# Kernel tuning notes

Hardware: AMD Instinct MI355X
Metric: run time of the kernel (lower is better)

## Reference

```python
import jax, jax.numpy as jnp
import numpy as np

N, L, E, H, D = 4, 2048, 1024, 16, 64

def setup_inputs() -> dict:
    key = jax.random.key(0)
    ks = jax.random.split(key, 8)
    s = 1.0 / np.sqrt(E)
    return {
        "Q": jax.random.normal(ks[0], (N, L, E), jnp.float32),
        "K": jax.random.normal(ks[1], (N, L, E), jnp.float32),
        "V": jax.random.normal(ks[2], (N, L, E), jnp.float32),
        "Wq": jax.random.normal(ks[3], (H * D, E), jnp.float32) * s,
        "bq": jnp.zeros((H * D,), jnp.float32),
        "Wk": jax.random.normal(ks[4], (H * D, E), jnp.float32) * s,
        "bk": jnp.zeros((H * D,), jnp.float32),
        "Wv": jax.random.normal(ks[5], (H * D, E), jnp.float32) * s,
        "bv": jnp.zeros((H * D,), jnp.float32),
        "Wo": jax.random.normal(ks[6], (E, H * D), jnp.float32) * s,
        "bo": jnp.zeros((E,), jnp.float32),
    }

def reference(Q, K, V, Wq, bq, Wk, bk, Wv, bv, Wo, bo):
    n, lq, e = Q.shape
    lk = K.shape[1]
    # projections: Linear(x) = x @ W.T + b
    q = (Q @ Wq.T + bq).reshape(n, lq, H, D)
    k = (K @ Wk.T + bk).reshape(n, lk, H, D)
    v = (V @ Wv.T + bv).reshape(n, lk, H, D)
    # scores over key dim (original broadcasts Q*K and sums over d)
    scores = jnp.einsum('nqhd,nkhd->nqkh', q, k) / jnp.sqrt(jnp.float32(D))
    attn = jax.nn.softmax(scores, axis=2)  # softmax over key axis
    out = jnp.einsum('nqkh,nkhd->nqhd', attn, v)
    out = out.reshape(n, lq, H * D)
    return (out @ Wo.T + bo).reshape(n, lq, E)
```

## Files before the change

### kernel.cpp

```cpp
#include <hip/hip_runtime.h>
#include <cstdint>
#include <cstddef>


typedef __bf16 bf16x8 __attribute__((ext_vector_type(8)));
typedef __bf16 bf16x4 __attribute__((ext_vector_type(4)));
typedef __bf16 bf16x2 __attribute__((ext_vector_type(2)));
typedef float f32x4 __attribute__((ext_vector_type(4)));
typedef float f32x2 __attribute__((ext_vector_type(2)));
typedef unsigned int uint2v __attribute__((ext_vector_type(2)));
typedef unsigned int uint4v __attribute__((ext_vector_type(4)));

#define LOG2E_OVER_SQRTD 0.18033688011112042f

__device__ __forceinline__ unsigned short f2bf(float f) {
  unsigned int u = __builtin_bit_cast(unsigned int, f);
  u = (u + 0x7fffu + ((u >> 16) & 1u)) >> 16;
  return (unsigned short)u;
}

__device__ __forceinline__ unsigned int pk2(float a, float b) {
  f32x2 t = {a, b};
  bf16x2 h = __builtin_convertvector(t, bf16x2);
  return __builtin_bit_cast(unsigned int, h);
}

__device__ __forceinline__ void gl2lds16(const void* g, void* l) {
  __builtin_amdgcn_global_load_lds(
      (__attribute__((address_space(1))) unsigned int*)g,
      (__attribute__((address_space(3))) unsigned int*)l, 16, 0, 0);
}

__device__ __forceinline__ bf16x8 mk_ap(f32x4 sA, f32x4 sB) {
  float peA[4], peB[4];
#pragma unroll
  for (int r = 0; r < 4; ++r) {
    peA[r] = __builtin_amdgcn_exp2f(sA[r]);
    peB[r] = __builtin_amdgcn_exp2f(sB[r]);
  }
  unsigned int x00 = pk2(peA[0], peA[1]);
  unsigned int x01 = pk2(peA[2], peA[3]);
  unsigned int x10 = pk2(peB[0], peB[1]);
  unsigned int x11 = pk2(peB[2], peB[3]);
  uint2v s0 = __builtin_amdgcn_permlane32_swap(x00, x10, false, false);
  uint2v t0 = __builtin_amdgcn_permlane16_swap(s0[0], s0[1], false, false);
  uint2v s1 = __builtin_amdgcn_permlane32_swap(x01, x11, false, false);
  uint2v t1 = __builtin_amdgcn_permlane16_swap(s1[0], s1[1], false, false);
  uint4v u;
  u[0] = t0[0];
  u[1] = t1[0];
  u[2] = t0[1];
  u[3] = t1[1];
  return __builtin_bit_cast(bf16x8, u);
}

struct CvtArgs {
  const float* src[7];
  unsigned short* dst[7];
};
__global__ __launch_bounds__(256) void cvt_all_k(CvtArgs a) {
  int bid = blockIdx.x;
  int which, x;
  if (bid < 24576) {
    which = bid >> 13;
    x = bid & 8191;
  } else {
    int r = bid - 24576;
    which = 3 + (r >> 10);
    x = r & 1023;
  }
  const float* s = a.src[which];
  unsigned short* d = a.dst[which];
  size_t i = ((size_t)x * 256 + threadIdx.x) * 4;
  float4 v = *(const float4*)(s + i);
  ushort4 o;
  o.x = f2bf(v.x); o.y = f2bf(v.y); o.z = f2bf(v.z); o.w = f2bf(v.w);
  *(ushort4*)(d + i) = o;
}

struct GemmDesc {
  const unsigned short* A;
  const unsigned short* Bt;
  const float* bias;
  void* C;
  int N;
  int nbx_shift;
  float scale;
  int bias_row;
  int permc;
};
struct GemmPack3 {
  GemmDesc g[3];
};

template <bool OUT_F32>
__global__ __launch_bounds__(256, 2) void gemm_multi_k(GemmPack3 p) {
  __shared__ __attribute__((aligned(16))) unsigned short As[128 * 64];
  __shared__ __attribute__((aligned(16))) unsigned short Bs[128 * 64];
  const GemmDesc d = p.g[blockIdx.x >> 9];
  const int t = blockIdx.x & 511;
  const int bx = t & ((1 << d.nbx_shift) - 1);
  const int by = t >> d.nbx_shift;

  const int tid = threadIdx.x;
  const int lane = tid & 63, wave = tid >> 6;
  const int lr = lane & 15, lg = lane >> 4;
  const int rowBase = by * 128;
  const int colBase = bx * 128;
  const int wm = (wave & 1) * 64, wn = (wave >> 1) * 64;

  f32x4 acc[4][4] = {};

  const unsigned short* gA[4];
  const unsigned short* gB[4];
  unsigned short* lA[4];
  unsigned short* lB[4];
#pragma unroll
  for (int i = 0; i < 4; ++i) {
    int s = tid + i * 256;
    int row = s >> 3;
    int c = (s & 7) ^ (row & 7);
    gA[i] = d.A + (size_t)(rowBase + row) * 1024 + c * 8;
    gB[i] = d.Bt + (size_t)(colBase + row) * 1024 + c * 8;
    lA[i] = &As[s * 8];
    lB[i] = &Bs[s * 8];
  }

  for (int kt = 0; kt < 16; ++kt) {
    const int ko = kt * 64;
#pragma unroll
    for (int i = 0; i < 4; ++i) {
      gl2lds16(gA[i] + ko, lA[i]);
      gl2lds16(gB[i] + ko, lB[i]);
    }
    __syncthreads();

#pragma unroll
    for (int ks = 0; ks < 2; ++ks) {
      bf16x8 af[4], bfr[4];
#pragma unroll
      for (int mt = 0; mt < 4; ++mt) {
        int row = wm + mt * 16 + lr;
        int c = (ks * 4 + lg) ^ (row & 7);
        af[mt] = *(const bf16x8*)&As[row * 64 + c * 8];
      }
#pragma unroll
      for (int nt = 0; nt < 4; ++nt) {
        int row = wn + nt * 16 + lr;
        int c = (ks * 4 + lg) ^ (row & 7);
        bfr[nt] = *(const bf16x8*)&Bs[row * 64 + c * 8];
      }
#pragma unroll
      for (int mt = 0; mt < 4; ++mt)
#pragma unroll
        for (int nt = 0; nt < 4; ++nt)
          acc[mt][nt] = __builtin_amdgcn_mfma_f32_16x16x32_bf16(
              af[mt], bfr[nt], acc[mt][nt], 0, 0, 0);
    }
    __syncthreads();
  }

#pragma unroll
  for (int mt = 0; mt < 4; ++mt)
#pragma unroll
    for (int nt = 0; nt < 4; ++nt) {
      int col = colBase + wn + nt * 16 + lr;
      int colStore = d.permc ? (colBase + wn + lr * 4 + nt) : col;
      float bcol = d.bias_row ? 0.f : d.bias[col];
#pragma unroll
      for (int r = 0; r < 4; ++r) {
        int row = rowBase + wm + mt * 16 + lg * 4 + r;
        float b = d.bias_row ? d.bias[row] : bcol;
        float val = (acc[mt][nt][r] + b) * d.scale;
        size_t idx = (size_t)row * (size_t)d.N + (size_t)colStore;
        if (OUT_F32)
          ((float*)d.C)[idx] = val;
        else
          ((unsigned short*)d.C)[idx] = f2bf(val);
      }
    }
}

__global__ __launch_bounds__(256, 4) void attn_k(
    const unsigned short* __restrict__ qb,
    const unsigned short* __restrict__ kb,
    const unsigned short* __restrict__ vtb,
    unsigned short* __restrict__ aob) {
  __shared__ __attribute__((aligned(16))) unsigned short Ks[2 * 64 * 64];
  __shared__ __attribute__((aligned(16))) unsigned short Vts[2 * 64 * 64];

  const int tid = threadIdx.x;
  const int lane = tid & 63, wave = tid >> 6;
  const int lr = lane & 15, lg = lane >> 4;

  const int bid = blockIdx.x;
  const int xcd = bid & 7;
  const int idx = bid >> 3;
  const int qt = idx & 15;
  const int nh = (idx >> 4) * 8 + xcd;
  const int h = nh & 15, n = nh >> 4;
  const int q0 = qt * 128;

#pragma unroll
  for (int i = 0; i < 4; ++i) {
    int s = i * 256 + tid;
    int row = s >> 3;
    int c = (s & 7) ^ (row & 7);
    gl2lds16(qb + (((size_t)n * 2048 + q0 + row) << 10) + h * 64 + c * 8,
             &Ks[s * 8]);
  }
  __syncthreads();

  bf16x8 aq[2][2];
#pragma unroll
  for (int mt = 0; mt < 2; ++mt)
#pragma unroll
    for (int ks = 0; ks < 2; ++ks) {
      int row = wave * 32 + mt * 16 + lr;
      int c = (ks * 4 + lg) ^ (row & 7);
      aq[mt][ks] = *(const bf16x8*)&Ks[row * 64 + c * 8];
    }
  __syncthreads();

  const int a0 = lr * 64 + ((lg ^ (lr & 7)) * 8);
  const int a1 = lr * 64 + (((4 + lg) ^ (lr & 7)) * 8);
  const unsigned short* Kb0 = &Ks[a0];
  const unsigned short* Kb1 = &Ks[a1];
  const unsigned short* Vb0 = &Vts[a0];
  const unsigned short* Vb1 = &Vts[a1];

  const unsigned short* kg[2];
  const unsigned short* vg[2];
  int ldo[2];
#pragma unroll
  for (int i = 0; i < 2; ++i) {
    int s = i * 256 + tid;
    int row = s >> 3;
    int c = (s & 7) ^ (row & 7);
    kg[i] = kb + (((size_t)n * 2048 + row) << 10) + h * 64 + c * 8;
    vg[i] = vtb + (((size_t)(h * 64 + row)) << 13) + (size_t)n * 2048 + c * 8;
    ldo[i] = s * 8;
  }
#pragma unroll
  for (int i = 0; i < 2; ++i) {
    gl2lds16(kg[i], &Ks[ldo[i]]);
    gl2lds16(vg[i], &Vts[ldo[i]]);
    kg[i] += 64 * 1024;
    vg[i] += 64;
  }

  bf16x8 ones;
#pragma unroll
  for (int i = 0; i < 8; ++i) ones[i] = (__bf16)1.0f;
  const f32x4 fzero = {0.f, 0.f, 0.f, 0.f};

  f32x4 o_acc[2][4] = {};
  f32x4 o_sum[2] = {};

#pragma unroll 2
  for (int kt = 0; kt < 32; ++kt) {
    const int cb = (kt & 1) * 4096;
    const int nb = 4096 - cb;
    __syncthreads();

    if (kt < 31) {
#pragma unroll
      for (int i = 0; i < 2; ++i) {
        gl2lds16(kg[i], &Ks[nb + ldo[i]]);
        gl2lds16(vg[i], &Vts[nb + ldo[i]]);
        kg[i] += 64 * 1024;
        vg[i] += 64;
      }
    }

    bf16x8 kf0[4], kf1[4];
#pragma unroll
    for (int nt = 0; nt < 4; ++nt) {
      kf0[nt] = *(const bf16x8*)(Kb0 + cb + nt * 1024);
      kf1[nt] = *(const bf16x8*)(Kb1 + cb + nt * 1024);
    }

    f32x4 sA[2][2], sB[2][2];
    __builtin_amdgcn_s_setprio(1);
#pragma unroll
    for (int mt = 0; mt < 2; ++mt)
#pragma unroll
      for (int nt = 0; nt < 2; ++nt) {
        f32x4 t0 = __builtin_amdgcn_mfma_f32_16x16x32_bf16(
            kf0[nt], aq[mt][0], fzero, 0, 0, 0);
        sA[mt][nt] = __builtin_amdgcn_mfma_f32_16x16x32_bf16(
            kf1[nt], aq[mt][1], t0, 0, 0, 0);
      }
#pragma unroll
    for (int mt = 0; mt < 2; ++mt)
#pragma unroll
      for (int nt = 0; nt < 2; ++nt) {
        f32x4 t0 = __builtin_amdgcn_mfma_f32_16x16x32_bf16(
            kf0[nt + 2], aq[mt][0], fzero, 0, 0, 0);
        sB[mt][nt] = __builtin_amdgcn_mfma_f32_16x16x32_bf16(
            kf1[nt + 2], aq[mt][1], t0, 0, 0, 0);
      }
    __builtin_amdgcn_s_setprio(0);

    bf16x8 bv0[4], bv1[4];
#pragma unroll
    for (int nt = 0; nt < 4; ++nt) {
      bv0[nt] = *(const bf16x8*)(Vb0 + cb + nt * 1024);
      bv1[nt] = *(const bf16x8*)(Vb1 + cb + nt * 1024);
    }

    bf16x8 ap0[2];
#pragma unroll
    for (int mt = 0; mt < 2; ++mt) ap0[mt] = mk_ap(sA[mt][0], sA[mt][1]);

    __builtin_amdgcn_s_setprio(1);
#pragma unroll
    for (int mt = 0; mt < 2; ++mt) {
      o_sum[mt] = __builtin_amdgcn_mfma_f32_16x16x32_bf16(
          ap0[mt], ones, o_sum[mt], 0, 0, 0);
#pragma unroll
      for (int nt = 0; nt < 4; ++nt)
        o_acc[mt][nt] = __builtin_amdgcn_mfma_f32_16x16x32_bf16(
            ap0[mt], bv0[nt], o_acc[mt][nt], 0, 0, 0);
    }
    __builtin_amdgcn_s_setprio(0);

    bf16x8 ap1[2];
#pragma unroll
    for (int mt = 0; mt < 2; ++mt) ap1[mt] = mk_ap(sB[mt][0], sB[mt][1]);

    __builtin_amdgcn_s_setprio(1);
#pragma unroll
    for (int mt = 0; mt < 2; ++mt) {
      o_sum[mt] = __builtin_amdgcn_mfma_f32_16x16x32_bf16(
          ap1[mt], ones, o_sum[mt], 0, 0, 0);
#pragma unroll
      for (int nt = 0; nt < 4; ++nt)
        o_acc[mt][nt] = __builtin_amdgcn_mfma_f32_16x16x32_bf16(
            ap1[mt], bv1[nt], o_acc[mt][nt], 0, 0, 0);
    }
    __builtin_amdgcn_s_setprio(0);
  }

#pragma unroll
  for (int mt = 0; mt < 2; ++mt) {
#pragma unroll
    for (int r = 0; r < 4; ++r) {
      float inv = 1.0f / o_sum[mt][r];
      int row_l = q0 + wave * 32 + mt * 16 + lg * 4 + r;
      size_t base = (((size_t)n * 2048 + row_l) << 10) + h * 64;
#pragma unroll
      for (int nt = 0; nt < 4; ++nt)
        aob[base + nt * 16 + lr] = f2bf(o_acc[mt][nt][r] * inv);
    }
  }
}

extern "C" void kernel_launch(void* const* d_in, const int* in_sizes, int n_in,
                              void* d_out, int out_size, void* d_ws,
                              size_t ws_size, hipStream_t stream) {
  const float* Q = (const float*)d_in[0];
  const float* K = (const float*)d_in[1];
  const float* V = (const float*)d_in[2];
  const float* Wq = (const float*)d_in[3];
  const float* bq = (const float*)d_in[4];
  const float* Wk = (const float*)d_in[5];
  const float* bk = (const float*)d_in[6];
  const float* Wv = (const float*)d_in[7];
  const float* bv = (const float*)d_in[8];
  const float* Wo = (const float*)d_in[9];
  const float* bo = (const float*)d_in[10];

  const size_t S = (size_t)8192 * 1024;
  const size_t W = (size_t)1024 * 1024;
  unsigned short* ws = (unsigned short*)d_ws;
  unsigned short* Qbf = ws;
  unsigned short* Kbf = ws + S;
  unsigned short* Vbf = ws + 2 * S;
  unsigned short* qbuf = ws + 3 * S;
  unsigned short* kbuf = ws + 4 * S;
  unsigned short* vtbuf = ws + 5 * S;
  unsigned short* Wqb = ws + 6 * S;
  unsigned short* Wkb = Wqb + W;
  unsigned short* Wvb = Wqb + 2 * W;
  unsigned short* Wob = Wqb + 3 * W;
  unsigned short* aob = Qbf;

  CvtArgs cv;
  cv.src[0] = Q;  cv.dst[0] = Qbf;
  cv.src[1] = K;  cv.dst[1] = Kbf;
  cv.src[2] = V;  cv.dst[2] = Vbf;
  cv.src[3] = Wq; cv.dst[3] = Wqb;
  cv.src[4] = Wk; cv.dst[4] = Wkb;
  cv.src[5] = Wv; cv.dst[5] = Wvb;
  cv.src[6] = Wo; cv.dst[6] = Wob;
  cvt_all_k<<<28672, 256, 0, stream>>>(cv);

  GemmPack3 pp;
  pp.g[0] = {Qbf, Wqb, bq, qbuf, 1024, 3, LOG2E_OVER_SQRTD, 0, 0};
  pp.g[1] = {Kbf, Wkb, bk, kbuf, 1024, 3, 1.0f, 0, 0};
  pp.g[2] = {Wvb, Vbf, bv, vtbuf, 8192, 6, 1.0f, 1, 0};
  gemm_multi_k<false><<<1536, 256, 0, stream>>>(pp);

  attn_k<<<1024, 256, 0, stream>>>(qbuf, kbuf, vtbuf, aob);

  GemmPack3 po;
  po.g[0] = {aob, Wob, bo, d_out, 1024, 3, 1.0f, 0, 0};
  po.g[1] = po.g[0];
  po.g[2] = po.g[0];
  gemm_multi_k<true><<<512, 256, 0, stream>>>(po);
}
```

Measured before the change: 361.2 us.

## Software-pipeline attention PV across iterations and compute row sums with VALU

Restructures the attention loop so the second half of P·V for the previous key tile is issued after the next tile's QK^T MFMAs. V now uses a triple-buffered LDS ring so the deferred tile stays resident. The softmax denominator is accumulated as per-lane float sums of the exponentials and reduced with shuffles, replacing the extra MFMA against a ones vector; these sums come from fp32 values rather than the bf16-rounded probabilities. The GEMM kernel also remaps block indices for the 8-column case to change tile traversal order for cache locality.

```diff
diff --git a/kernel.cpp b/kernel.cpp
--- a/kernel.cpp
+++ b/kernel.cpp
@@ -31,13 +31,15 @@
       (__attribute__((address_space(3))) unsigned int*)l, 16, 0, 0);
 }
 
-__device__ __forceinline__ bf16x8 mk_ap(f32x4 sA, f32x4 sB) {
+__device__ __forceinline__ bf16x8 mk_ap(f32x4 sA, f32x4 sB, float& lsum) {
   float peA[4], peB[4];
 #pragma unroll
   for (int r = 0; r < 4; ++r) {
     peA[r] = __builtin_amdgcn_exp2f(sA[r]);
     peB[r] = __builtin_amdgcn_exp2f(sB[r]);
   }
+  lsum += ((peA[0] + peA[1]) + (peA[2] + peA[3])) +
+          ((peB[0] + peB[1]) + (peB[2] + peB[3]));
   unsigned int x00 = pk2(peA[0], peA[1]);
   unsigned int x01 = pk2(peA[2], peA[3]);
   unsigned int x10 = pk2(peB[0], peB[1]);
@@ -98,7 +100,8 @@
   __shared__ __attribute__((aligned(16))) unsigned short As[128 * 64];
   __shared__ __attribute__((aligned(16))) unsigned short Bs[128 * 64];
   const GemmDesc d = p.g[blockIdx.x >> 9];
-  const int t = blockIdx.x & 511;
+  int t = blockIdx.x & 511;
+  if (d.nbx_shift == 3) t = ((t & 7) << 6) | (t >> 3);
   const int bx = t & ((1 << d.nbx_shift) - 1);
   const int by = t >> d.nbx_shift;
 
@@ -187,7 +190,7 @@
     const unsigned short* __restrict__ vtb,
     unsigned short* __restrict__ aob) {
   __shared__ __attribute__((aligned(16))) unsigned short Ks[2 * 64 * 64];
-  __shared__ __attribute__((aligned(16))) unsigned short Vts[2 * 64 * 64];
+  __shared__ __attribute__((aligned(16))) unsigned short Vts[3 * 64 * 64];
 
   const int tid = threadIdx.x;
   const int lane = tid & 63, wave = tid >> 6;
@@ -201,34 +204,6 @@
   const int h = nh & 15, n = nh >> 4;
   const int q0 = qt * 128;
 
-#pragma unroll
-  for (int i = 0; i < 4; ++i) {
-    int s = i * 256 + tid;
-    int row = s >> 3;
-    int c = (s & 7) ^ (row & 7);
-    gl2lds16(qb + (((size_t)n * 2048 + q0 + row) << 10) + h * 64 + c * 8,
-             &Ks[s * 8]);
-  }
-  __syncthreads();
-
-  bf16x8 aq[2][2];
-#pragma unroll
-  for (int mt = 0; mt < 2; ++mt)
-#pragma unroll
-    for (int ks = 0; ks < 2; ++ks) {
-      int row = wave * 32 + mt * 16 + lr;
-      int c = (ks * 4 + lg) ^ (row & 7);
-      aq[mt][ks] = *(const bf16x8*)&Ks[row * 64 + c * 8];
-    }
-  __syncthreads();
-
-  const int a0 = lr * 64 + ((lg ^ (lr & 7)) * 8);
-  const int a1 = lr * 64 + (((4 + lg) ^ (lr & 7)) * 8);
-  const unsigned short* Kb0 = &Ks[a0];
-  const unsigned short* Kb1 = &Ks[a1];
-  const unsigned short* Vb0 = &Vts[a0];
-  const unsigned short* Vb1 = &Vts[a1];
-
   const unsigned short* kg[2];
   const unsigned short* vg[2];
   int ldo[2];
@@ -241,112 +216,171 @@
     vg[i] = vtb + (((size_t)(h * 64 + row)) << 13) + (size_t)n * 2048 + c * 8;
     ldo[i] = s * 8;
   }
+
+#pragma unroll
+  for (int i = 0; i < 2; ++i) {
+    gl2lds16(vg[i], &Vts[ldo[i]]);
+    gl2lds16(vg[i] + 64, &Vts[4096 + ldo[i]]);
+    vg[i] += 128;
+  }
+#pragma unroll
+  for (int i = 0; i < 4; ++i) {
+    int s = i * 256 + tid;
+    int row = s >> 3;
+    int c = (s & 7) ^ (row & 7);
+    gl2lds16(qb + (((size_t)n * 2048 + q0 + row) << 10) + h * 64 + c * 8,
+             &Ks[s * 8]);
+  }
+  __syncthreads();
+
+  bf16x8 aq[2][2];
+#pragma unroll
+  for (int mt = 0; mt < 2; ++mt)
+#pragma unroll
+    for (int ks = 0; ks < 2; ++ks) {
+      int row = wave * 32 + mt * 16 + lr;
+      int c = (ks * 4 + lg) ^ (row & 7);
+      aq[mt][ks] = *(const bf16x8*)&Ks[row * 64 + c * 8];
+    }
+  __syncthreads();
+
 #pragma unroll
   for (int i = 0; i < 2; ++i) {
     gl2lds16(kg[i], &Ks[ldo[i]]);
-    gl2lds16(vg[i], &Vts[ldo[i]]);
-    kg[i] += 64 * 1024;
-    vg[i] += 64;
-  }
-
-  bf16x8 ones;
-#pragma unroll
-  for (int i = 0; i < 8; ++i) ones[i] = (__bf16)1.0f;
+    kg[i] += 65536;
+  }
+
+  const int a0 = lr * 64 + ((lg ^ (lr & 7)) * 8);
+  const int a1 = lr * 64 + (((4 + lg) ^ (lr & 7)) * 8);
+  const unsigned short* Kb0 = &Ks[a0];
+  const unsigned short* Kb1 = &Ks[a1];
+  const unsigned short* Vb0 = &Vts[a0];
+  const unsigned short* Vb1 = &Vts[a1];
+
   const f32x4 fzero = {0.f, 0.f, 0.f, 0.f};
-
   f32x4 o_acc[2][4] = {};
-  f32x4 o_sum[2] = {};
+  float lsum[2] = {};
+  bf16x8 ap_prev[2];
+  int vp = 8192, vc = 0, vn = 4096;
+
+  f32x4 sA[2][2], sB[2][2];
+
+#define QKT(cb)                                                            \
+  {                                                                        \
+    bf16x8 kf[4];                                                          \
+    _Pragma("unroll") for (int nt = 0; nt < 4; ++nt) kf[nt] =              \
+        *(const bf16x8*)(Kb0 + (cb) + nt * 1024);                          \
+    __builtin_amdgcn_s_setprio(1);                                         \
+    _Pragma("unroll") for (int mt = 0; mt < 2; ++mt) {                     \
+      sA[mt][0] = __builtin_amdgcn_mfma_f32_16x16x32_bf16(kf[0], aq[mt][0],\
+                                                          fzero, 0, 0, 0); \
+      sA[mt][1] = __builtin_amdgcn_mfma_f32_16x16x32_bf16(kf[1], aq[mt][0],\
+                                                          fzero, 0, 0, 0); \
+      sB[mt][0] = __builtin_amdgcn_mfma_f32_16x16x32_bf16(kf[2], aq[mt][0],\
+                                                          fzero, 0, 0, 0); \
+      sB[mt][1] = __builtin_amdgcn_mfma_f32_16x16x32_bf16(kf[3], aq[mt][0],\
+                                                          fzero, 0, 0, 0); \
+    }                                                                      \
+    __builtin_amdgcn_s_setprio(0);                                         \
+  }                                                                        \
+  {                                                                        \
+    bf16x8 kf[4];                                                          \
+    _Pragma("unroll") for (int nt = 0; nt < 4; ++nt) kf[nt] =              \
+        *(const bf16x8*)(Kb1 + (cb) + nt * 1024);                          \
+    __builtin_amdgcn_s_setprio(1);                                         \
+    _Pragma("unroll") for (int mt = 0; mt < 2; ++mt) {                     \
+      sA[mt][0] = __builtin_amdgcn_mfma_f32_16x16x32_bf16(                 \
+          kf[0], aq[mt][1], sA[mt][0], 0, 0, 0);                           \
+      sA[mt][1] = __builtin_amdgcn_mfma_f32_16x16x32_bf16(                 \
+          kf[1], aq[mt][1], sA[mt][1], 0, 0, 0);                           \
+      sB[mt][0] = __builtin_amdgcn_mfma_f32_16x16x32_bf16(                 \
+          kf[2], aq[mt][1], sB[mt][0], 0, 0, 0);                           \
+      sB[mt][1] = __builtin_amdgcn_mfma_f32_16x16x32_bf16(                 \
+          kf[3], aq[mt][1], sB[mt][1], 0, 0, 0);                           \
+    }                                                                      \
+    __builtin_amdgcn_s_setprio(0);                                         \
+  }
+
+#define PVH(apv, VBASE, voff)                                              \
+  {                                                                        \
+    bf16x8 bv[4];                                                          \
+    _Pragma("unroll") for (int nt = 0; nt < 4; ++nt) bv[nt] =              \
+        *(const bf16x8*)((VBASE) + (voff) + nt * 1024);                    \
+    __builtin_amdgcn_s_setprio(1);                                         \
+    _Pragma("unroll") for (int mt = 0; mt < 2; ++mt)                       \
+        _Pragma("unroll") for (int nt = 0; nt < 4; ++nt) o_acc[mt][nt] =   \
+            __builtin_amdgcn_mfma_f32_16x16x32_bf16(apv[mt], bv[nt],       \
+                                                    o_acc[mt][nt], 0, 0, 0);\
+    __builtin_amdgcn_s_setprio(0);                                         \
+  }
+
+  {
+    __syncthreads();
+#pragma unroll
+    for (int i = 0; i < 2; ++i) {
+      gl2lds16(kg[i], &Ks[4096 + ldo[i]]);
+      kg[i] += 65536;
+    }
+    QKT(0)
+    bf16x8 ap0[2];
+#pragma unroll
+    for (int mt = 0; mt < 2; ++mt) ap0[mt] = mk_ap(sA[mt][0], sA[mt][1], lsum[mt]);
+    PVH(ap0, Vb0, vc)
+#pragma unroll
+    for (int mt = 0; mt < 2; ++mt)
+      ap_prev[mt] = mk_ap(sB[mt][0], sB[mt][1], lsum[mt]);
+    int t = vp; vp = vc; vc = vn; vn = t;
+  }
 
 #pragma unroll 2
-  for (int kt = 0; kt < 32; ++kt) {
+  for (int kt = 1; kt < 31; ++kt) {
     const int cb = (kt & 1) * 4096;
     const int nb = 4096 - cb;
     __syncthreads();
-
-    if (kt < 31) {
-#pragma unroll
-      for (int i = 0; i < 2; ++i) {
-        gl2lds16(kg[i], &Ks[nb + ldo[i]]);
-        gl2lds16(vg[i], &Vts[nb + ldo[i]]);
-        kg[i] += 64 * 1024;
-        vg[i] += 64;
-      }
-    }
-
-    bf16x8 kf0[4], kf1[4];
-#pragma unroll
-    for (int nt = 0; nt < 4; ++nt) {
-      kf0[nt] = *(const bf16x8*)(Kb0 + cb + nt * 1024);
-      kf1[nt] = *(const bf16x8*)(Kb1 + cb + nt * 1024);
-    }
-
-    f32x4 sA[2][2], sB[2][2];
-    __builtin_amdgcn_s_setprio(1);
+#pragma unroll
+    for (int i = 0; i < 2; ++i) {
+      gl2lds16(kg[i], &Ks[nb + ldo[i]]);
+      gl2lds16(vg[i], &Vts[vn + ldo[i]]);
+      kg[i] += 65536;
+      vg[i] += 64;
+    }
+    QKT(cb)
+    PVH(ap_prev, Vb1, vp)
+    bf16x8 ap0[2];
+#pragma unroll
+    for (int mt = 0; mt < 2; ++mt) ap0[mt] = mk_ap(sA[mt][0], sA[mt][1], lsum[mt]);
+    PVH(ap0, Vb0, vc)
 #pragma unroll
     for (int mt = 0; mt < 2; ++mt)
-#pragma unroll
-      for (int nt = 0; nt < 2; ++nt) {
-        f32x4 t0 = __builtin_amdgcn_mfma_f32_16x16x32_bf16(
-            kf0[nt], aq[mt][0], fzero, 0, 0, 0);
-        sA[mt][nt] = __builtin_amdgcn_mfma_f32_16x16x32_bf16(
-            kf1[nt], aq[mt][1], t0, 0, 0, 0);
-      }
+      ap_prev[mt] = mk_ap(sB[mt][0], sB[mt][1], lsum[mt]);
+    int t = vp; vp = vc; vc = vn; vn = t;
+  }
+
+  {
+    __syncthreads();
+    QKT(4096)
+    PVH(ap_prev, Vb1, vp)
+    bf16x8 ap0[2];
+#pragma unroll
+    for (int mt = 0; mt < 2; ++mt) ap0[mt] = mk_ap(sA[mt][0], sA[mt][1], lsum[mt]);
+    PVH(ap0, Vb0, vc)
 #pragma unroll
     for (int mt = 0; mt < 2; ++mt)
-#pragma unroll
-      for (int nt = 0; nt < 2; ++nt) {
-        f32x4 t0 = __builtin_amdgcn_mfma_f32_16x16x32_bf16(
-            kf0[nt + 2], aq[mt][0], fzero, 0, 0, 0);
-        sB[mt][nt] = __builtin_amdgcn_mfma_f32_16x16x32_bf16(
-            kf1[nt + 2], aq[mt][1], t0, 0, 0, 0);
-      }
-    __builtin_amdgcn_s_setprio(0);
-
-    bf16x8 bv0[4], bv1[4];
-#pragma unroll
-    for (int nt = 0; nt < 4; ++nt) {
-      bv0[nt] = *(const bf16x8*)(Vb0 + cb + nt * 1024);
-      bv1[nt] = *(const bf16x8*)(Vb1 + cb + nt * 1024);
-    }
-
-    bf16x8 ap0[2];
-#pragma unroll
-    for (int mt = 0; mt < 2; ++mt) ap0[mt] = mk_ap(sA[mt][0], sA[mt][1]);
-
-    __builtin_amdgcn_s_setprio(1);
-#pragma unroll
-    for (int mt = 0; mt < 2; ++mt) {
-      o_sum[mt] = __builtin_amdgcn_mfma_f32_16x16x32_bf16(
-          ap0[mt], ones, o_sum[mt], 0, 0, 0);
-#pragma unroll
-      for (int nt = 0; nt < 4; ++nt)
-        o_acc[mt][nt] = __builtin_amdgcn_mfma_f32_16x16x32_bf16(
-            ap0[mt], bv0[nt], o_acc[mt][nt], 0, 0, 0);
-    }
-    __builtin_amdgcn_s_setprio(0);
-
-    bf16x8 ap1[2];
-#pragma unroll
-    for (int mt = 0; mt < 2; ++mt) ap1[mt] = mk_ap(sB[mt][0], sB[mt][1]);
-
-    __builtin_amdgcn_s_setprio(1);
-#pragma unroll
-    for (int mt = 0; mt < 2; ++mt) {
-      o_sum[mt] = __builtin_amdgcn_mfma_f32_16x16x32_bf16(
-          ap1[mt], ones, o_sum[mt], 0, 0, 0);
-#pragma unroll
-      for (int nt = 0; nt < 4; ++nt)
-        o_acc[mt][nt] = __builtin_amdgcn_mfma_f32_16x16x32_bf16(
-            ap1[mt], bv1[nt], o_acc[mt][nt], 0, 0, 0);
-    }
-    __builtin_amdgcn_s_setprio(0);
-  }
+      ap_prev[mt] = mk_ap(sB[mt][0], sB[mt][1], lsum[mt]);
+    PVH(ap_prev, Vb1, vc)
+  }
+#undef QKT
+#undef PVH
 
 #pragma unroll
   for (int mt = 0; mt < 2; ++mt) {
+    float l = lsum[mt];
+    l += __shfl_xor(l, 16);
+    l += __shfl_xor(l, 32);
 #pragma unroll
     for (int r = 0; r < 4; ++r) {
-      float inv = 1.0f / o_sum[mt][r];
+      float lv = __shfl(l, lg * 4 + r);
+      float inv = 1.0f / lv;
       int row_l = q0 + wave * 32 + mt * 16 + lg * 4 + r;
       size_t base = (((size_t)n * 2048 + row_l) << 10) + h * 64;
 #pragma unroll
```

Result: slower. 430.4 us (+19.2%).

## Use two waves per attention block with 64 query rows each; swizzle GEMM tiles

Applied to the files above, without the earlier changes.

The attention kernel now runs 128 threads (2 waves) per block. Each wave owns 64 query rows instead of 32, so every K/V fragment read from LDS feeds twice as many MFMAs, and the main loop is restructured into two halves per key tile. This cuts LDS read traffic per MFMA but raises register pressure and halves the number of waves per block for latency hiding. Separately, the GEMM kernel's launch-bounds occupancy rises to 3 and its tile index is swizzled for the 8-column-tile cases, aiming at better cache locality.

```diff
diff --git a/kernel.cpp b/kernel.cpp
--- a/kernel.cpp
+++ b/kernel.cpp
@@ -94,11 +94,12 @@
 };
 
 template <bool OUT_F32>
-__global__ __launch_bounds__(256, 2) void gemm_multi_k(GemmPack3 p) {
+__global__ __launch_bounds__(256, 3) void gemm_multi_k(GemmPack3 p) {
   __shared__ __attribute__((aligned(16))) unsigned short As[128 * 64];
   __shared__ __attribute__((aligned(16))) unsigned short Bs[128 * 64];
   const GemmDesc d = p.g[blockIdx.x >> 9];
-  const int t = blockIdx.x & 511;
+  int t = blockIdx.x & 511;
+  if (d.nbx_shift == 3) t = ((t & 7) << 6) | (t >> 3);
   const int bx = t & ((1 << d.nbx_shift) - 1);
   const int by = t >> d.nbx_shift;
 
@@ -181,7 +182,7 @@
     }
 }
 
-__global__ __launch_bounds__(256, 4) void attn_k(
+__global__ __launch_bounds__(128, 2) void attn_k(
     const unsigned short* __restrict__ qb,
     const unsigned short* __restrict__ kb,
     const unsigned short* __restrict__ vtb,
@@ -202,8 +203,8 @@
   const int q0 = qt * 128;
 
 #pragma unroll
-  for (int i = 0; i < 4; ++i) {
-    int s = i * 256 + tid;
+  for (int i = 0; i < 8; ++i) {
+    int s = i * 128 + tid;
     int row = s >> 3;
     int c = (s & 7) ^ (row & 7);
     gl2lds16(qb + (((size_t)n * 2048 + q0 + row) << 10) + h * 64 + c * 8,
@@ -211,12 +212,12 @@
   }
   __syncthreads();
 
-  bf16x8 aq[2][2];
-#pragma unroll
-  for (int mt = 0; mt < 2; ++mt)
+  bf16x8 aq[4][2];
+#pragma unroll
+  for (int mt = 0; mt < 4; ++mt)
 #pragma unroll
     for (int ks = 0; ks < 2; ++ks) {
-      int row = wave * 32 + mt * 16 + lr;
+      int row = wave * 64 + mt * 16 + lr;
       int c = (ks * 4 + lg) ^ (row & 7);
       aq[mt][ks] = *(const bf16x8*)&Ks[row * 64 + c * 8];
     }
@@ -229,12 +230,12 @@
   const unsigned short* Vb0 = &Vts[a0];
   const unsigned short* Vb1 = &Vts[a1];
 
-  const unsigned short* kg[2];
-  const unsigned short* vg[2];
-  int ldo[2];
-#pragma unroll
-  for (int i = 0; i < 2; ++i) {
-    int s = i * 256 + tid;
+  const unsigned short* kg[4];
+  const unsigned short* vg[4];
+  int ldo[4];
+#pragma unroll
+  for (int i = 0; i < 4; ++i) {
+    int s = i * 128 + tid;
     int row = s >> 3;
     int c = (s & 7) ^ (row & 7);
     kg[i] = kb + (((size_t)n * 2048 + row) << 10) + h * 64 + c * 8;
@@ -242,7 +243,7 @@
     ldo[i] = s * 8;
   }
 #pragma unroll
-  for (int i = 0; i < 2; ++i) {
+  for (int i = 0; i < 4; ++i) {
     gl2lds16(kg[i], &Ks[ldo[i]]);
     gl2lds16(vg[i], &Vts[ldo[i]]);
     kg[i] += 64 * 1024;
@@ -254,10 +255,9 @@
   for (int i = 0; i < 8; ++i) ones[i] = (__bf16)1.0f;
   const f32x4 fzero = {0.f, 0.f, 0.f, 0.f};
 
-  f32x4 o_acc[2][4] = {};
-  f32x4 o_sum[2] = {};
-
-#pragma unroll 2
+  f32x4 o_acc[4][4] = {};
+  f32x4 o_sum[4] = {};
+
   for (int kt = 0; kt < 32; ++kt) {
     const int cb = (kt & 1) * 4096;
     const int nb = 4096 - cb;
@@ -265,7 +265,7 @@
 
     if (kt < 31) {
 #pragma unroll
-      for (int i = 0; i < 2; ++i) {
+      for (int i = 0; i < 4; ++i) {
         gl2lds16(kg[i], &Ks[nb + ldo[i]]);
         gl2lds16(vg[i], &Vts[nb + ldo[i]]);
         kg[i] += 64 * 1024;
@@ -273,81 +273,59 @@
       }
     }
 
-    bf16x8 kf0[4], kf1[4];
-#pragma unroll
-    for (int nt = 0; nt < 4; ++nt) {
-      kf0[nt] = *(const bf16x8*)(Kb0 + cb + nt * 1024);
-      kf1[nt] = *(const bf16x8*)(Kb1 + cb + nt * 1024);
-    }
-
-    f32x4 sA[2][2], sB[2][2];
-    __builtin_amdgcn_s_setprio(1);
-#pragma unroll
-    for (int mt = 0; mt < 2; ++mt)
-#pragma unroll
-      for (int nt = 0; nt < 2; ++nt) {
-        f32x4 t0 = __builtin_amdgcn_mfma_f32_16x16x32_bf16(
-            kf0[nt], aq[mt][0], fzero, 0, 0, 0);
-        sA[mt][nt] = __builtin_amdgcn_mfma_f32_16x16x32_bf16(
-            kf1[nt], aq[mt][1], t0, 0, 0, 0);
-      }
-#pragma unroll
-    for (int mt = 0; mt < 2; ++mt)
-#pragma unroll
-      for (int nt = 0; nt < 2; ++nt) {
-        f32x4 t0 = __builtin_amdgcn_mfma_f32_16x16x32_bf16(
-            kf0[nt + 2], aq[mt][0], fzero, 0, 0, 0);
-        sB[mt][nt] = __builtin_amdgcn_mfma_f32_16x16x32_bf16(
-            kf1[nt + 2], aq[mt][1], t0, 0, 0, 0);
-      }
-    __builtin_amdgcn_s_setprio(0);
-
-    bf16x8 bv0[4], bv1[4];
-#pragma unroll
-    for (int nt = 0; nt < 4; ++nt) {
-      bv0[nt] = *(const bf16x8*)(Vb0 + cb + nt * 1024);
-      bv1[nt] = *(const bf16x8*)(Vb1 + cb + nt * 1024);
-    }
-
-    bf16x8 ap0[2];
-#pragma unroll
-    for (int mt = 0; mt < 2; ++mt) ap0[mt] = mk_ap(sA[mt][0], sA[mt][1]);
-
-    __builtin_amdgcn_s_setprio(1);
-#pragma unroll
-    for (int mt = 0; mt < 2; ++mt) {
-      o_sum[mt] = __builtin_amdgcn_mfma_f32_16x16x32_bf16(
-          ap0[mt], ones, o_sum[mt], 0, 0, 0);
+#pragma unroll
+    for (int half = 0; half < 2; ++half) {
+      const int ko = half * 2048;
+      f32x4 s0[4], s1[4];
+      {
+        bf16x8 k00 = *(const bf16x8*)(Kb0 + cb + ko);
+        bf16x8 k10 = *(const bf16x8*)(Kb1 + cb + ko);
+        bf16x8 k01 = *(const bf16x8*)(Kb0 + cb + ko + 1024);
+        bf16x8 k11 = *(const bf16x8*)(Kb1 + cb + ko + 1024);
+        __builtin_amdgcn_s_setprio(1);
+#pragma unroll
+        for (int mt = 0; mt < 4; ++mt) {
+          f32x4 t0 = __builtin_amdgcn_mfma_f32_16x16x32_bf16(
+              k00, aq[mt][0], fzero, 0, 0, 0);
+          s0[mt] = __builtin_amdgcn_mfma_f32_16x16x32_bf16(
+              k10, aq[mt][1], t0, 0, 0, 0);
+          f32x4 t1 = __builtin_amdgcn_mfma_f32_16x16x32_bf16(
+              k01, aq[mt][0], fzero, 0, 0, 0);
+          s1[mt] = __builtin_amdgcn_mfma_f32_16x16x32_bf16(
+              k11, aq[mt][1], t1, 0, 0, 0);
+        }
+        __builtin_amdgcn_s_setprio(0);
+      }
+      const unsigned short* vb = half ? Vb1 : Vb0;
+      bf16x8 bv[4];
 #pragma unroll
       for (int nt = 0; nt < 4; ++nt)
-        o_acc[mt][nt] = __builtin_amdgcn_mfma_f32_16x16x32_bf16(
-            ap0[mt], bv0[nt], o_acc[mt][nt], 0, 0, 0);
-    }
-    __builtin_amdgcn_s_setprio(0);
-
-    bf16x8 ap1[2];
-#pragma unroll
-    for (int mt = 0; mt < 2; ++mt) ap1[mt] = mk_ap(sB[mt][0], sB[mt][1]);
-
-    __builtin_amdgcn_s_setprio(1);
-#pragma unroll
-    for (int mt = 0; mt < 2; ++mt) {
-      o_sum[mt] = __builtin_amdgcn_mfma_f32_16x16x32_bf16(
-          ap1[mt], ones, o_sum[mt], 0, 0, 0);
-#pragma unroll
-      for (int nt = 0; nt < 4; ++nt)
-        o_acc[mt][nt] = __builtin_amdgcn_mfma_f32_16x16x32_bf16(
-            ap1[mt], bv1[nt], o_acc[mt][nt], 0, 0, 0);
-    }
-    __builtin_amdgcn_s_setprio(0);
-  }
-
-#pragma unroll
-  for (int mt = 0; mt < 2; ++mt) {
+        bv[nt] = *(const bf16x8*)(vb + cb + nt * 1024);
+
+      bf16x8 ap[4];
+#pragma unroll
+      for (int mt = 0; mt < 4; ++mt) ap[mt] = mk_ap(s0[mt], s1[mt]);
+
+      __builtin_amdgcn_s_setprio(1);
+#pragma unroll
+      for (int mt = 0; mt < 4; ++mt) {
+        o_sum[mt] = __builtin_amdgcn_mfma_f32_16x16x32_bf16(
+            ap[mt], ones, o_sum[mt], 0, 0, 0);
+#pragma unroll
+        for (int nt = 0; nt < 4; ++nt)
+          o_acc[mt][nt] = __builtin_amdgcn_mfma_f32_16x16x32_bf16(
+              ap[mt], bv[nt], o_acc[mt][nt], 0, 0, 0);
+      }
+      __builtin_amdgcn_s_setprio(0);
+    }
+  }
+
+#pragma unroll
+  for (int mt = 0; mt < 4; ++mt) {
 #pragma unroll
     for (int r = 0; r < 4; ++r) {
       float inv = 1.0f / o_sum[mt][r];
-      int row_l = q0 + wave * 32 + mt * 16 + lg * 4 + r;
+      int row_l = q0 + wave * 64 + mt * 16 + lg * 4 + r;
       size_t base = (((size_t)n * 2048 + row_l) << 10) + h * 64;
 #pragma unroll
       for (int nt = 0; nt < 4; ++nt)
@@ -402,7 +380,7 @@
   pp.g[2] = {Wvb, Vbf, bv, vtbuf, 8192, 6, 1.0f, 1, 0};
   gemm_multi_k<false><<<1536, 256, 0, stream>>>(pp);
 
-  attn_k<<<1024, 256, 0, stream>>>(qbuf, kbuf, vtbuf, aob);
+  attn_k<<<1024, 128, 0, stream>>>(qbuf, kbuf, vtbuf, aob);
 
   GemmPack3 po;
   po.g[0] = {aob, Wob, bo, d_out, 1024, 3, 1.0f, 0, 0};
```

Measured after the change: 339.4 us. 1.06x faster.
